# Performance work log

Measured on AMD Instinct MI355X. Metric: run time of the kernel, lower is better.

Reference implementation:

```python
import jax, jax.numpy as jnp
import numpy as np

N = 200000      # nodes
E = 6400000     # edges (avg degree 32)
F_IN = 4        # node feature dim used by GraphConv
H = 184         # 4 * scale(46)
MD_H = 16       # min_distance MLP width
L1 = 188        # H + 4
A = 5           # action_space


def _uniform(k, shape, fan_in):
    b = 1.0 / np.sqrt(fan_in)
    return jax.random.uniform(k, shape, jnp.float32, -b, b)


def setup_inputs() -> dict:
    key = jax.random.key(0)
    ks = jax.random.split(key, 16)
    node_feat = jax.random.normal(ks[0], (N, 6), jnp.float32)
    edge_index = jax.random.randint(ks[1], (2, E), 0, N, dtype=jnp.int32)
    edge_weight = jax.random.uniform(ks[2], (E,), jnp.float32)
    center_idx = 0
    return {
        "node_feat": node_feat,
        "edge_index": edge_index,
        "edge_weight": edge_weight,
        "center_idx": center_idx,
        # GraphConv(4, 184): lin_rel (with bias) applied to aggregated msgs, lin_root (no bias) to x
        "W_rel": _uniform(ks[3], (F_IN, H), F_IN),
        "b_rel": _uniform(ks[4], (H,), F_IN),
        "W_root": _uniform(ks[5], (F_IN, H), F_IN),
        # linear2: 2 -> 16
        "W2": _uniform(ks[6], (2, MD_H), 2),
        "b2": _uniform(ks[7], (MD_H,), 2),
        # linear2_1: 16 -> 16
        "W21": _uniform(ks[8], (MD_H, MD_H), MD_H),
        "b21": _uniform(ks[9], (MD_H,), MD_H),
        # linear1: 200 -> 188
        "W1": _uniform(ks[10], (H + MD_H, L1), H + MD_H),
        "b1": _uniform(ks[11], (L1,), H + MD_H),
        # linear4: 188 -> 5
        "W4": _uniform(ks[12], (L1, A), L1),
        "b4": _uniform(ks[13], (A,), L1),
    }


def reference(node_feat, edge_index, edge_weight, center_idx,
              W_rel, b_rel, W_root, W2, b2, W21, b21, W1, b1, W4, b4):
    x = node_feat[:, :4]                                   # [N, 4]
    src, dst = edge_index[0], edge_index[1]
    # GraphConv message: e_ji * x_j, mean-aggregated at target nodes
    msg = x[src] * edge_weight[:, None]                    # [E, 4]
    agg = jax.ops.segment_sum(msg, dst, num_segments=N)    # [N, 4]
    deg = jax.ops.segment_sum(jnp.ones((E,), jnp.float32), dst, num_segments=N)
    mean = agg / jnp.maximum(deg, 1.0)[:, None]
    h = jax.nn.relu(mean @ W_rel + b_rel + x @ W_root)     # [N, 184]
    # global_max_pool with batch=None -> max over all nodes
    x1 = jnp.max(h, axis=0, keepdims=True)                 # [1, 184]
    x2 = h[center_idx:center_idx + 1]                      # [1, 184]
    g = x2 - x1
    md = node_feat[center_idx, 4:].reshape(1, 2)           # [1, 2]
    md = jax.nn.relu(md @ W2 + b2)
    md = jax.nn.relu(md @ W21 + b21)
    g = jnp.concatenate([g, md], axis=1)                   # [1, 200]
    g = jax.nn.relu(g @ W1 + b1)
    return g @ W4 + b4                                     # [1, 5]
```

## Files before the change

### kernel.cpp

```cpp
#include <hip/hip_runtime.h>

#define H 184
#define MDH 16
#define L1D 188
#define BBITS 9
#define BSZ 512
#define KMAX 512
#define CHUNKE 4096
#define SSUB 4
#define SREC_CAP 4416
#define RPT 9
#define NSPLIT 4

__global__ void zero_kernel(int* __restrict__ p, int n) {
    int i = blockIdx.x * blockDim.x + threadIdx.x;
    if (i < n) p[i] = 0;
}

__global__ __launch_bounds__(256) void pack_kernel(
        const float* __restrict__ nf, float4* __restrict__ x4,
        int* __restrict__ zp, int zn, int N) {
    __shared__ float s[256 * 6];
    int base = blockIdx.x * 256;
    int t = threadIdx.x;
    if (blockIdx.x == 0 && zp != nullptr)
        for (int i = t; i < zn; i += 256) zp[i] = 0;
    for (int i = t; i < 256 * 6; i += 256) {
        int gi = base * 6 + i;
        s[i] = (gi < N * 6) ? nf[gi] : 0.0f;
    }
    __syncthreads();
    int n = base + t;
    if (n < N)
        x4[n] = make_float4(s[t * 6], s[t * 6 + 1], s[t * 6 + 2], s[t * 6 + 3]);
}

__device__ __forceinline__ void scan512_w8(const int* __restrict__ cnt,
                                           int* __restrict__ sc,
                                           int* __restrict__ wtot, int t) {
    int wv = t >> 6, ln = t & 63;
    int x = cnt[t];
    #pragma unroll
    for (int d = 1; d < 64; d <<= 1) {
        int y = __shfl_up(x, d, 64);
        if (ln >= d) x += y;
    }
    if (ln == 63) wtot[wv] = x;
    __syncthreads();
    int woff = 0;
    #pragma unroll
    for (int wq = 0; wq < 7; ++wq) woff += (wq < wv) ? wtot[wq] : 0;
    sc[t] = woff + x;
    __syncthreads();
}

__global__ __launch_bounds__(512, 8) void partition_cs_kernel(
        const int* __restrict__ ei, const float* __restrict__ ew,
        int* __restrict__ cursor, uint2* __restrict__ region,
        int E, int K, int CAP) {
    __shared__ uint2 srec[CHUNKE];
    __shared__ int cnt[KMAX];
    __shared__ int sc[KMAX];
    __shared__ int wbase[KMAX];
    __shared__ int wtot[8];
    int t = threadIdx.x;
    int c = blockIdx.x;

    int e0 = c * CHUNKE;
    int e1 = min(E, e0 + CHUNKE);

    cnt[t] = 0;
    __syncthreads();

    unsigned meta[8];
    unsigned srcv[8];
    unsigned wv[8];
    #pragma unroll
    for (int j = 0; j < 2; ++j) {
        int e = e0 + t * 4 + j * 2048;
        int4 d4 = make_int4(0, 0, 0, 0);
        int4 s4 = make_int4(0, 0, 0, 0);
        float4 w4 = make_float4(0.f, 0.f, 0.f, 0.f);
        bool full = (e + 3 < e1);
        if (full) {
            d4 = *(const int4*)(ei + E + e);
            s4 = *(const int4*)(ei + e);
            w4 = *(const float4*)(ew + e);
        }
        #pragma unroll
        for (int q = 0; q < 4; ++q) {
            int idx = j * 4 + q;
            meta[idx] = 0xFFFFFFFFu;
            int eq = e + q;
            if (eq < e1) {
                int dst = full ? (q == 0 ? d4.x : q == 1 ? d4.y : q == 2 ? d4.z : d4.w)
                               : ei[E + eq];
                int src = full ? (q == 0 ? s4.x : q == 1 ? s4.y : q == 2 ? s4.z : s4.w)
                               : ei[eq];
                float w = full ? (q == 0 ? w4.x : q == 1 ? w4.y : q == 2 ? w4.z : w4.w)
                               : ew[eq];
                int k = ((unsigned)dst) >> BBITS;
                int r = atomicAdd(&cnt[k], 1);
                meta[idx] = ((unsigned)k << 21) | ((unsigned)r << 9)
                          | ((unsigned)dst & (BSZ - 1));
                srcv[idx] = (unsigned)src;
                wv[idx]   = __float_as_uint(w);
            }
        }
    }
    __syncthreads();

    scan512_w8(cnt, sc, wtot, t);

    {
        int ck = cnt[t];
        int pos = sc[t] - ck;
        int b = 0;
        if (t < K && ck > 0) {
            b = atomicAdd(&cursor[t], ck);
            if (b + ck > CAP) b = CAP - ck;
        }
        wbase[t] = b;
        cnt[t] = pos;
    }
    __syncthreads();

    #pragma unroll
    for (int j = 0; j < 8; ++j) {
        if (meta[j] != 0xFFFFFFFFu) {
            int k  = meta[j] >> 21;
            int r  = (meta[j] >> 9) & 0xFFF;
            int dl = meta[j] & (BSZ - 1);
            int slot = cnt[k] + r;
            srec[slot] = make_uint2(((unsigned)dl << 18) | srcv[j], wv[j]);
        }
    }
    __syncthreads();

    {
        int pos = cnt[t];
        int ck = sc[t] - pos;
        if (t < K && ck > 0) {
            uint2* dstp = region + (size_t)t * CAP + wbase[t];
            for (int i = 0; i < ck; ++i)
                dstp[i] = srec[pos + i];
        }
    }
}

__global__ __launch_bounds__(512, 8) void bucket_sort_accum_kernel(
        const float4* __restrict__ x4, const uint2* __restrict__ region,
        const int* __restrict__ cursor, float* __restrict__ partials, int CAP) {
    __shared__ uint2 srec[SREC_CAP];
    __shared__ int cnt[BSZ], sc[BSZ];
    __shared__ int wtot[8];
    int k = blockIdx.x / SSUB;
    int s = blockIdx.x % SSUB;
    int t = threadIdx.x;

    cnt[t] = 0;
    __syncthreads();

    int len = cursor[k];
    if (len > CAP) len = CAP;
    const uint2* base = region + (size_t)k * CAP;
    int i0 = (int)(((long long)len * s) / SSUB);
    int i1 = (int)(((long long)len * (s + 1)) / SSUB);

    uint2 rec[RPT];
    unsigned rb[RPT];
    #pragma unroll
    for (int j = 0; j < RPT; ++j) {
        int i = i0 + t + j * 512;
        rb[j] = 0xFFFFFFFFu;
        if (i < i1) {
            uint2 r = base[i];
            int bin = r.x >> 18;
            int rk = atomicAdd(&cnt[bin], 1);
            rec[j] = r;
            rb[j] = ((unsigned)bin << 13) | (unsigned)rk;
        }
    }
    __syncthreads();

    scan512_w8(cnt, sc, wtot, t);

    #pragma unroll
    for (int j = 0; j < RPT; ++j) {
        if (rb[j] != 0xFFFFFFFFu) {
            int bin = rb[j] >> 13;
            int rk  = rb[j] & 0x1FFF;
            int slot = sc[bin] - cnt[bin] + rk;
            srec[slot] = rec[j];
        }
    }
    __syncthreads();

    int cA = cnt[t], startA = sc[t] - cA;
    float4 aA = make_float4(0.f, 0.f, 0.f, 0.f);
    for (int i = 0; i < cA; ++i) {
        uint2 r = srec[startA + i];
        float4 xv = x4[r.x & 0x3FFFFu];
        float w = __uint_as_float(r.y);
        aA.x += xv.x * w; aA.y += xv.y * w;
        aA.z += xv.z * w; aA.w += xv.w * w;
    }
    float* pp = partials + (size_t)blockIdx.x * (BSZ * 5);
    pp[0 * BSZ + t] = aA.x;
    pp[1 * BSZ + t] = aA.y;
    pp[2 * BSZ + t] = aA.z;
    pp[3 * BSZ + t] = aA.w;
    pp[4 * BSZ + t] = (float)cA;
}

__global__ __launch_bounds__(256) void edge_atomic_kernel(
        const float* __restrict__ nf, const int* __restrict__ ei,
        const float* __restrict__ ew, float* __restrict__ agg,
        float* __restrict__ deg, int E) {
    int e = blockIdx.x * blockDim.x + threadIdx.x;
    if (e >= E) return;
    int src = ei[e];
    int dst = ei[E + e];
    float w = ew[e];
    const float2* xr = (const float2*)(nf + (size_t)src * 6);
    float2 x01 = xr[0];
    float2 x23 = xr[1];
    float* a = agg + (size_t)dst * 4;
    atomicAdd(a + 0, x01.x * w);
    atomicAdd(a + 1, x01.y * w);
    atomicAdd(a + 2, x23.x * w);
    atomicAdd(a + 3, x23.y * w);
    atomicAdd(deg + dst, 1.0f);
}

__global__ __launch_bounds__(256) void node_bucket_kernel(
        const float4* __restrict__ x4,
        const float* __restrict__ partials,
        const float* __restrict__ W_rel, const float* __restrict__ b_rel,
        const float* __restrict__ W_root,
        const int*   __restrict__ centerp,
        unsigned int* __restrict__ xmax_bits,
        float* __restrict__ h0,
        int N) {
    __shared__ float4 xm[BSZ / NSPLIT];
    __shared__ float4 xt[BSZ / NSPLIT];
    const int NB = BSZ / NSPLIT;
    int k = blockIdx.x / NSPLIT;
    int q = blockIdx.x % NSPLIT;
    int t = threadIdx.x;
    int center = *centerp;
    int base_d = q * NB;
    int nmax = min(BSZ, N - (k << BBITS));
    int cnt_local = min(NB, nmax - base_d);
    if (cnt_local <= 0) return;
    const float* bp = partials + (size_t)k * SSUB * (BSZ * 5);

    if (t < NB) {
        int d = base_d + t;
        float a0 = 0.f, a1 = 0.f, a2 = 0.f, a3 = 0.f, dg = 0.f;
        #pragma unroll
        for (int s = 0; s < SSUB; ++s) {
            const float* p = bp + (size_t)s * (BSZ * 5);
            a0 += p[0 * BSZ + d];
            a1 += p[1 * BSZ + d];
            a2 += p[2 * BSZ + d];
            a3 += p[3 * BSZ + d];
            dg += p[4 * BSZ + d];
        }
        float inv = 1.0f / fmaxf(dg, 1.0f);
        xm[t] = make_float4(a0 * inv, a1 * inv, a2 * inv, a3 * inv);
    } else {
        int i = t - NB;
        int n = (k << BBITS) + base_d + i;
        xt[i] = (n < N) ? x4[n] : make_float4(0.f, 0.f, 0.f, 0.f);
    }
    __syncthreads();

    int j = t;
    if (j >= H) return;

    float wr0 = W_rel[0 * H + j], wr1 = W_rel[1 * H + j];
    float wr2 = W_rel[2 * H + j], wr3 = W_rel[3 * H + j];
    float wo0 = W_root[0 * H + j], wo1 = W_root[1 * H + j];
    float wo2 = W_root[2 * H + j], wo3 = W_root[3 * H + j];
    float b = b_rel[j];

    int cd = ((center >> BBITS) == k) ? (center & (BSZ - 1)) - base_d : -1;
    float mx = 0.0f;
    for (int i = 0; i < cnt_local; ++i) {
        float4 m = xm[i];
        float4 x = xt[i];
        float v = b
                + m.x * wr0 + m.y * wr1 + m.z * wr2 + m.w * wr3
                + x.x * wo0 + x.y * wo1 + x.z * wo2 + x.w * wo3;
        v = fmaxf(v, 0.0f);
        mx = fmaxf(mx, v);
        if (i == cd) h0[j] = v;
    }
    atomicMax(xmax_bits + j, __float_as_uint(mx));
}

__global__ __launch_bounds__(192) void node_kernel(
        const float4* __restrict__ x4,
        const float* __restrict__ agg,
        const float* __restrict__ deg,
        const float* __restrict__ W_rel, const float* __restrict__ b_rel,
        const float* __restrict__ W_root,
        const int*   __restrict__ centerp,
        unsigned int* __restrict__ xmax_bits,
        float* __restrict__ h0,
        int N, int nodes_per_block) {
    int j = threadIdx.x;
    if (j >= H) return;
    int center = *centerp;
    int n0 = blockIdx.x * nodes_per_block;
    int n1 = n0 + nodes_per_block;
    if (n1 > N) n1 = N;

    float wr0 = W_rel[0 * H + j], wr1 = W_rel[1 * H + j];
    float wr2 = W_rel[2 * H + j], wr3 = W_rel[3 * H + j];
    float wo0 = W_root[0 * H + j], wo1 = W_root[1 * H + j];
    float wo2 = W_root[2 * H + j], wo3 = W_root[3 * H + j];
    float b = b_rel[j];

    float mx = 0.0f;
    for (int n = n0; n < n1; ++n) {
        float4 a = ((const float4*)agg)[n];
        float inv = 1.0f / fmaxf(deg[n], 1.0f);
        float4 x = x4[n];
        float v = b
                + (a.x * inv) * wr0 + (a.y * inv) * wr1
                + (a.z * inv) * wr2 + (a.w * inv) * wr3
                + x.x * wo0 + x.y * wo1 + x.z * wo2 + x.w * wo3;
        v = fmaxf(v, 0.0f);
        mx = fmaxf(mx, v);
        if (n == center) h0[j] = v;
    }
    atomicMax(xmax_bits + j, __float_as_uint(mx));
}

__global__ __launch_bounds__(768) void final_kernel(
        const float* __restrict__ nf,
        const int*   __restrict__ centerp,
        const unsigned int* __restrict__ xmax_bits,
        const float* __restrict__ h0,
        const float* __restrict__ W2,  const float* __restrict__ b2,
        const float* __restrict__ W21, const float* __restrict__ b21,
        const float* __restrict__ W1,  const float* __restrict__ b1,
        const float* __restrict__ W4,  const float* __restrict__ b4,
        float* __restrict__ out) {
    __shared__ float gin[H + MDH];
    __shared__ float md0[MDH];
    __shared__ float part[4][L1D];
    __shared__ float g1[L1D];
    int t = threadIdx.x;
    int center = *centerp;

    if (t < H) gin[t] = h0[t] - __uint_as_float(xmax_bits[t]);
    if (t < MDH) {
        float m0 = nf[(size_t)center * 6 + 4];
        float m1 = nf[(size_t)center * 6 + 5];
        md0[t] = fmaxf(m0 * W2[t] + m1 * W2[MDH + t] + b2[t], 0.0f);
    }
    __syncthreads();
    if (t < MDH) {
        float s = b21[t];
        for (int k = 0; k < MDH; ++k) s += md0[k] * W21[k * MDH + t];
        gin[H + t] = fmaxf(s, 0.0f);
    }
    __syncthreads();

    {
        int kc = t / 192;
        int j  = t - kc * 192;
        if (j < L1D) {
            float s = 0.0f;
            int k0 = kc * 50, k1 = k0 + 50;
            #pragma unroll 5
            for (int k = k0; k < k1; ++k) s += gin[k] * W1[k * L1D + j];
            part[kc][j] = s;
        }
    }
    __syncthreads();
    if (t < L1D)
        g1[t] = fmaxf(part[0][t] + part[1][t] + part[2][t] + part[3][t] + b1[t],
                      0.0f);
    __syncthreads();

    int w = t >> 6, ln = t & 63;
    if (w < 5) {
        float s = 0.0f;
        for (int k = ln; k < L1D; k += 64) s += g1[k] * W4[k * 5 + w];
        #pragma unroll
        for (int d = 32; d > 0; d >>= 1) s += __shfl_down(s, d, 64);
        if (ln == 0) out[w] = s + b4[w];
    }
}

extern "C" void kernel_launch(void* const* d_in, const int* in_sizes, int n_in,
                              void* d_out, int out_size, void* d_ws, size_t ws_size,
                              hipStream_t stream) {
    const float* nf      = (const float*)d_in[0];
    const int*   ei      = (const int*)  d_in[1];
    const float* ew      = (const float*)d_in[2];
    const int*   centerp = (const int*)  d_in[3];
    const float* W_rel   = (const float*)d_in[4];
    const float* b_rel   = (const float*)d_in[5];
    const float* W_root  = (const float*)d_in[6];
    const float* W2      = (const float*)d_in[7];
    const float* b2      = (const float*)d_in[8];
    const float* W21     = (const float*)d_in[9];
    const float* b21     = (const float*)d_in[10];
    const float* W1      = (const float*)d_in[11];
    const float* b1      = (const float*)d_in[12];
    const float* W4      = (const float*)d_in[13];
    const float* b4      = (const float*)d_in[14];
    float* out = (float*)d_out;

    const int N = in_sizes[0] / 6;
    const int E = in_sizes[1] / 2;
    const int K = (N + BSZ - 1) >> BBITS;
    const int nchunks = (E + CHUNKE - 1) / CHUNKE;
    int cap = E / K + E / K / 16 + 256;
    cap = (cap + 63) & ~63;

    int*          cursor   = (int*)d_ws;
    unsigned int* xmax     = (unsigned int*)(cursor + 512);
    float*        h0       = (float*)(xmax + H);
    float*        agg      = h0 + H;
    float*        deg      = agg + (size_t)N * 4;
    float4*       x4       = (float4*)(deg + N);
    float*        partials = (float*)(x4 + N);
    uint2*        region   = (uint2*)(partials + (size_t)K * SSUB * (BSZ * 5));

    size_t need = (size_t)((char*)(region + (size_t)K * cap) - (char*)d_ws);
    bool fast = (ws_size >= need) && (K <= KMAX) && (N <= (1 << 18))
             && ((E & 3) == 0)
             && ((cap + SSUB - 1) / SSUB <= SREC_CAP);

    if (fast) {
        pack_kernel<<<(N + 255) / 256, 256, 0, stream>>>(nf, x4, cursor, 512 + H, N);
        partition_cs_kernel<<<nchunks, 512, 0, stream>>>(ei, ew, cursor, region,
                                                         E, K, cap);
        bucket_sort_accum_kernel<<<K * SSUB, 512, 0, stream>>>(x4, region, cursor,
                                                               partials, cap);
        node_bucket_kernel<<<K * NSPLIT, 256, 0, stream>>>(x4, partials,
                                                           W_rel, b_rel, W_root,
                                                           centerp, xmax, h0, N);
    } else {
        const int blocks = 2048;
        const int npb = (N + blocks - 1) / blocks;
        zero_kernel<<<(N * 5 + 255) / 256, 256, 0, stream>>>((int*)agg, N * 5);
        zero_kernel<<<1, 256, 0, stream>>>(cursor, 512 + H);
        pack_kernel<<<(N + 255) / 256, 256, 0, stream>>>(nf, x4, nullptr, 0, N);
        edge_atomic_kernel<<<(E + 255) / 256, 256, 0, stream>>>(nf, ei, ew, agg, deg, E);
        node_kernel<<<blocks, 192, 0, stream>>>(x4, agg, deg,
                                                W_rel, b_rel, W_root,
                                                centerp, xmax, h0, N, npb);
    }

    final_kernel<<<1, 768, 0, stream>>>(nf, centerp, xmax, h0,
                                        W2, b2, W21, b21, W1, b1, W4, b4, out);
}
```

Baseline: 273.3 us.

## Fuse node packing into partition kernel and pre-multiply gathered features before bucket sort

The x4 packing step moves into the first npack blocks of the partition kernel, and the cursor/xmax zeroing becomes a hipMemsetAsync, which removes one kernel launch. The bucket accumulate kernel now gathers x4 and multiplies by the edge weight before the local sort. It processes the span in two halves and stores float4 weighted features in shared memory, so the reduction is a plain sum from LDS instead of a gather per sorted record. This issues the random gathers earlier and with more memory-level parallelism, in exchange for twice the sync and scan passes and larger shared-memory records.

```diff
diff --git a/kernel.cpp b/kernel.cpp
--- a/kernel.cpp
+++ b/kernel.cpp
@@ -9,7 +9,8 @@
 #define CHUNKE 4096
 #define SSUB 4
 #define SREC_CAP 4416
-#define RPT 9
+#define HREC 2240
+#define HRPT 5
 #define NSPLIT 4
 
 __global__ void zero_kernel(int* __restrict__ p, int n) {
@@ -57,7 +58,8 @@
 __global__ __launch_bounds__(512, 8) void partition_cs_kernel(
         const int* __restrict__ ei, const float* __restrict__ ew,
         int* __restrict__ cursor, uint2* __restrict__ region,
-        int E, int K, int CAP) {
+        const float* __restrict__ nf, float4* __restrict__ x4,
+        int E, int K, int CAP, int N, int npack) {
     __shared__ uint2 srec[CHUNKE];
     __shared__ int cnt[KMAX];
     __shared__ int sc[KMAX];
@@ -65,6 +67,22 @@
     __shared__ int wtot[8];
     int t = threadIdx.x;
     int c = blockIdx.x;
+
+    if (c < npack) {
+        float* sp = (float*)srec;
+        int base = c * 256;
+        for (int i = t; i < 256 * 6; i += 512) {
+            int gi = base * 6 + i;
+            sp[i] = (gi < N * 6) ? nf[gi] : 0.0f;
+        }
+        __syncthreads();
+        if (t < 256) {
+            int n = base + t;
+            if (n < N)
+                x4[n] = make_float4(sp[t * 6], sp[t * 6 + 1],
+                                    sp[t * 6 + 2], sp[t * 6 + 3]);
+        }
+    }
 
     int e0 = c * CHUNKE;
     int e1 = min(E, e0 + CHUNKE);
@@ -151,66 +169,75 @@
 __global__ __launch_bounds__(512, 8) void bucket_sort_accum_kernel(
         const float4* __restrict__ x4, const uint2* __restrict__ region,
         const int* __restrict__ cursor, float* __restrict__ partials, int CAP) {
-    __shared__ uint2 srec[SREC_CAP];
+    __shared__ float4 sxw[HREC];
     __shared__ int cnt[BSZ], sc[BSZ];
     __shared__ int wtot[8];
     int k = blockIdx.x / SSUB;
     int s = blockIdx.x % SSUB;
     int t = threadIdx.x;
 
-    cnt[t] = 0;
-    __syncthreads();
-
     int len = cursor[k];
     if (len > CAP) len = CAP;
     const uint2* base = region + (size_t)k * CAP;
     int i0 = (int)(((long long)len * s) / SSUB);
     int i1 = (int)(((long long)len * (s + 1)) / SSUB);
-
-    uint2 rec[RPT];
-    unsigned rb[RPT];
+    int span = i1 - i0;
+
+    float4 acc = make_float4(0.f, 0.f, 0.f, 0.f);
+    int degc = 0;
+
     #pragma unroll
-    for (int j = 0; j < RPT; ++j) {
-        int i = i0 + t + j * 512;
-        rb[j] = 0xFFFFFFFFu;
-        if (i < i1) {
-            uint2 r = base[i];
-            int bin = r.x >> 18;
-            int rk = atomicAdd(&cnt[bin], 1);
-            rec[j] = r;
-            rb[j] = ((unsigned)bin << 13) | (unsigned)rk;
-        }
-    }
-    __syncthreads();
-
-    scan512_w8(cnt, sc, wtot, t);
-
-    #pragma unroll
-    for (int j = 0; j < RPT; ++j) {
-        if (rb[j] != 0xFFFFFFFFu) {
-            int bin = rb[j] >> 13;
-            int rk  = rb[j] & 0x1FFF;
-            int slot = sc[bin] - cnt[bin] + rk;
-            srec[slot] = rec[j];
-        }
-    }
-    __syncthreads();
-
-    int cA = cnt[t], startA = sc[t] - cA;
-    float4 aA = make_float4(0.f, 0.f, 0.f, 0.f);
-    for (int i = 0; i < cA; ++i) {
-        uint2 r = srec[startA + i];
-        float4 xv = x4[r.x & 0x3FFFFu];
-        float w = __uint_as_float(r.y);
-        aA.x += xv.x * w; aA.y += xv.y * w;
-        aA.z += xv.z * w; aA.w += xv.w * w;
-    }
+    for (int half = 0; half < 2; ++half) {
+        int h0 = i0 + (span * half) / 2;
+        int h1 = i0 + (span * (half + 1)) / 2;
+        cnt[t] = 0;
+        __syncthreads();
+
+        float4 xw[HRPT];
+        unsigned rb[HRPT];
+        #pragma unroll
+        for (int j = 0; j < HRPT; ++j) {
+            int i = h0 + t + j * 512;
+            rb[j] = 0xFFFFFFFFu;
+            if (i < h1) {
+                uint2 r = base[i];
+                int bin = r.x >> 18;
+                float4 xv = x4[r.x & 0x3FFFFu];
+                float w = __uint_as_float(r.y);
+                xw[j] = make_float4(xv.x * w, xv.y * w, xv.z * w, xv.w * w);
+                int rk = atomicAdd(&cnt[bin], 1);
+                rb[j] = ((unsigned)bin << 13) | (unsigned)rk;
+            }
+        }
+        __syncthreads();
+
+        scan512_w8(cnt, sc, wtot, t);
+
+        #pragma unroll
+        for (int j = 0; j < HRPT; ++j) {
+            if (rb[j] != 0xFFFFFFFFu) {
+                int bin = rb[j] >> 13;
+                int rk  = rb[j] & 0x1FFF;
+                sxw[sc[bin] - cnt[bin] + rk] = xw[j];
+            }
+        }
+        __syncthreads();
+
+        int c = cnt[t], st = sc[t] - c;
+        for (int i = 0; i < c; ++i) {
+            float4 v = sxw[st + i];
+            acc.x += v.x; acc.y += v.y; acc.z += v.z; acc.w += v.w;
+        }
+        degc += c;
+        __syncthreads();
+    }
+
     float* pp = partials + (size_t)blockIdx.x * (BSZ * 5);
-    pp[0 * BSZ + t] = aA.x;
-    pp[1 * BSZ + t] = aA.y;
-    pp[2 * BSZ + t] = aA.z;
-    pp[3 * BSZ + t] = aA.w;
-    pp[4 * BSZ + t] = (float)cA;
+    pp[0 * BSZ + t] = acc.x;
+    pp[1 * BSZ + t] = acc.y;
+    pp[2 * BSZ + t] = acc.z;
+    pp[3 * BSZ + t] = acc.w;
+    pp[4 * BSZ + t] = (float)degc;
 }
 
 __global__ __launch_bounds__(256) void edge_atomic_kernel(
@@ -421,6 +448,7 @@
     const int E = in_sizes[1] / 2;
     const int K = (N + BSZ - 1) >> BBITS;
     const int nchunks = (E + CHUNKE - 1) / CHUNKE;
+    const int npack = (N + 255) / 256;
     int cap = E / K + E / K / 16 + 256;
     cap = (cap + 63) & ~63;
 
@@ -436,12 +464,15 @@
     size_t need = (size_t)((char*)(region + (size_t)K * cap) - (char*)d_ws);
     bool fast = (ws_size >= need) && (K <= KMAX) && (N <= (1 << 18))
              && ((E & 3) == 0)
-             && ((cap + SSUB - 1) / SSUB <= SREC_CAP);
+             && ((cap + SSUB - 1) / SSUB <= SREC_CAP)
+             && (((cap + SSUB - 1) / SSUB + 1) / 2 <= HREC)
+             && (npack <= nchunks);
 
     if (fast) {
-        pack_kernel<<<(N + 255) / 256, 256, 0, stream>>>(nf, x4, cursor, 512 + H, N);
+        hipMemsetAsync(cursor, 0, (size_t)(512 + H) * sizeof(int), stream);
         partition_cs_kernel<<<nchunks, 512, 0, stream>>>(ei, ew, cursor, region,
-                                                         E, K, cap);
+                                                         nf, x4, E, K, cap,
+                                                         N, npack);
         bucket_sort_accum_kernel<<<K * SSUB, 512, 0, stream>>>(x4, region, cursor,
                                                                partials, cap);
         node_bucket_kernel<<<K * NSPLIT, 256, 0, stream>>>(x4, partials,
```

Result: no change. 270.1 us (-1.2%).
